# Kernel optimization log

Measured on AMD Instinct MI355X. Metric: run time of the kernel, lower is better.

## Reference

```python
import math
import jax, jax.numpy as jnp
import numpy as np

B, S, D, H, DFF, BASE = 2, 2048, 1024, 16, 4096, 10000.0
HD = D // H  # 64


def setup_inputs() -> dict:
    key = jax.random.key(0)
    ks = jax.random.split(key, 16)
    sc = 0.02
    inp = {
        "x": jax.random.normal(ks[0], (B, S, D), jnp.float32),
        "positions": jnp.arange(S, dtype=jnp.int32),
        "wq": jax.random.normal(ks[1], (D, D), jnp.float32) * sc,
        "bq": jnp.zeros((D,), jnp.float32),
        "wk": jax.random.normal(ks[2], (D, D), jnp.float32) * sc,
        "bk": jnp.zeros((D,), jnp.float32),
        "wv": jax.random.normal(ks[3], (D, D), jnp.float32) * sc,
        "bv": jnp.zeros((D,), jnp.float32),
        "wo": jax.random.normal(ks[4], (D, D), jnp.float32) * sc,
        "bo": jnp.zeros((D,), jnp.float32),
        "phase_bias": jax.random.uniform(ks[5], (H, HD), jnp.float32, -2.0 * math.pi, 0.0),
        "w1": jax.random.normal(ks[6], (D, DFF), jnp.float32) * sc,
        "b1": jnp.zeros((DFF,), jnp.float32),
        "w2": jax.random.normal(ks[7], (DFF, D), jnp.float32) * sc,
        "b2": jnp.zeros((D,), jnp.float32),
        "g1": jnp.ones((D,), jnp.float32),
        "be1": jnp.zeros((D,), jnp.float32),
        "g2": jnp.ones((D,), jnp.float32),
        "be2": jnp.zeros((D,), jnp.float32),
    }
    return inp


def _layernorm(x, g, b):
    mu = jnp.mean(x, -1, keepdims=True)
    var = jnp.mean(jnp.square(x - mu), -1, keepdims=True)
    return (x - mu) / jnp.sqrt(var + 1e-5) * g + b


def _block(x, positions, wq, bq, wk, bk, wv, bv, wo, bo, phase_bias,
           w1, b1, w2, b2, g1, be1, g2, be2):
    # projections -> (B, H, S, HD)
    def heads(w, b):
        return (x @ w + b).reshape(B, S, H, HD).transpose(0, 2, 1, 3)
    q, k, v = heads(wq, bq), heads(wk, bk), heads(wv, bv)

    # PoPE: magnitudes via softplus, phases from position*freq (+ clamped bias for k)
    mu_q = jax.nn.softplus(q)
    mu_k = jax.nn.softplus(k)
    freqs = 1.0 / BASE ** (jnp.arange(HD, dtype=jnp.float32) / HD)      # (HD,)
    pos_ph = positions[:, None].astype(jnp.float32) * freqs[None, :]     # (S, HD)
    q_ph = pos_ph[None, None]                                            # (1,1,S,HD)
    cb = jnp.clip(phase_bias, -2.0 * math.pi, 0.0)
    k_ph = pos_ph[None, None] + cb[None, :, None, :]                     # (1,H,S,HD)
    q_p = jnp.concatenate([mu_q * jnp.cos(q_ph), mu_q * jnp.sin(q_ph)], -1)  # (B,H,S,2HD)
    k_p = jnp.concatenate([mu_k * jnp.cos(k_ph), mu_k * jnp.sin(k_ph)], -1)

    # manual attention with causal mask and softmax1
    scale = 1.0 / math.sqrt(2 * HD)
    scores = jnp.einsum("bhqd,bhkd->bhqk", q_p, k_p) * scale
    causal = jnp.triu(jnp.ones((S, S), bool), 1)
    scores = jnp.where(causal, -jnp.inf, scores)
    m = jnp.max(scores, -1, keepdims=True)  # finite: diagonal always unmasked
    e = jnp.exp(scores - m)
    w = e / (jnp.exp(-m) + jnp.sum(e, -1, keepdims=True))
    attn = jnp.einsum("bhqk,bhkd->bhqd", w, v)
    attn = attn.transpose(0, 2, 1, 3).reshape(B, S, D) @ wo + bo

    h = _layernorm(x + attn, g1, be1)
    ff = jax.nn.relu(h @ w1 + b1) @ w2 + b2
    return _layernorm(h + ff, g2, be2)


def reference(x, positions, wq, bq, wk, bk, wv, bv, wo, bo, phase_bias,
              w1, b1, w2, b2, g1, be1, g2, be2):
    return _block(x, positions, wq, bq, wk, bk, wv, bv, wo, bo, phase_bias,
                  w1, b1, w2, b2, g1, be1, g2, be2)
```

## Files before the change

### kernel.cpp

```cpp
#include <hip/hip_runtime.h>
#include <hip/hip_bf16.h>
#include <math.h>

#define NB 2
#define NS 2048
#define ND 1024
#define NH 16
#define NHD 64
#define NDFF 4096

typedef __attribute__((ext_vector_type(4))) float f32x4;
typedef __attribute__((ext_vector_type(8))) short bf16x8;

__device__ __forceinline__ short f2bf(float f) {
  union { float f; unsigned u; } v; v.f = f;
  unsigned r = v.u + 0x7fffu + ((v.u >> 16) & 1u);
  return (short)(r >> 16);
}
__device__ __forceinline__ float bf2f(unsigned short u) {
  union { unsigned u; float f; } v; v.u = ((unsigned)u) << 16; return v.f;
}
__device__ __forceinline__ float softplus_f(float x) {
  return fmaxf(x, 0.f) + log1pf(__expf(-fabsf(x)));
}
__device__ __forceinline__ void gl16(const short* g, short* l) {
  __builtin_amdgcn_global_load_lds(
      (const __attribute__((address_space(1))) void*)g,
      (__attribute__((address_space(3))) void*)l, 16, 0, 0);
}
__device__ __forceinline__ void xcd_map(int& row0, int& col0) {
  const int gx = gridDim.x, gy = gridDim.y;
  const int bid = blockIdx.y * gx + blockIdx.x;
  const int rows_px = gy >> 3;
  const int xcd = bid & 7, l = bid >> 3;
  row0 = (xcd * rows_px + (l % rows_px)) * 128;
  col0 = (l / rows_px) * 128;
}

__global__ __launch_bounds__(256) void k_wt(const float* __restrict__ W,
    short* __restrict__ Wt, int K, int N) {
  __shared__ float t[64][65];
  const int k0 = blockIdx.y * 64, n0 = blockIdx.x * 64;
  for (int i = threadIdx.x; i < 4096; i += 256) {
    const int r = i >> 6, c = i & 63;
    t[r][c] = W[(size_t)(k0 + r) * N + n0 + c];
  }
  __syncthreads();
  for (int i = threadIdx.x; i < 4096; i += 256) {
    const int r = i >> 6, c = i & 63;
    Wt[(size_t)(n0 + r) * K + k0 + c] = f2bf(t[c][r]);
  }
}

__global__ __launch_bounds__(256) void k_xb(const float* __restrict__ x,
    short* __restrict__ xb, int n8) {
  const int i = blockIdx.x * 256 + threadIdx.x;
  if (i >= n8) return;
  const float4 a = ((const float4*)x)[i * 2];
  const float4 b = ((const float4*)x)[i * 2 + 1];
  short tmp[8] = { f2bf(a.x), f2bf(a.y), f2bf(a.z), f2bf(a.w),
                   f2bf(b.x), f2bf(b.y), f2bf(b.z), f2bf(b.w) };
  *(int4*)&xb[(size_t)i * 8] = *(const int4*)tmp;
}

__global__ __launch_bounds__(256) void k_prep_v(const short* __restrict__ vb,
    short* __restrict__ vt) {
  __shared__ short t[64][72];
  const int bh = blockIdx.y, b = bh >> 4, h = bh & 15;
  const int s0 = blockIdx.x * 64;
  for (int i = threadIdx.x; i < 512; i += 256) {
    const int sl = i >> 3, d8 = (i & 7) * 8;
    int4 vv = *(const int4*)&vb[((size_t)(b * NS + s0 + sl) * NH + h) * NHD + d8];
    const short* sp = (const short*)&vv;
#pragma unroll
    for (int j = 0; j < 8; j++) t[d8 + j][sl] = sp[j];
  }
  __syncthreads();
  for (int i = threadIdx.x; i < 512; i += 256) {
    const int d = i >> 3, c8 = (i & 7) * 8;
    *(int4*)&vt[((size_t)bh * 64 + d) * NS + s0 + c8] = *(const int4*)&t[d][c8];
  }
}

__global__ __launch_bounds__(256) void k_pope(const short* __restrict__ qb,
    const short* __restrict__ kb, const int* __restrict__ positions,
    const float* __restrict__ phb, short* __restrict__ qp,
    short* __restrict__ kp) {
  const size_t i8 = ((size_t)blockIdx.x * 256 + threadIdx.x) * 8;
  const int d0 = (int)(i8 & 63);
  const int h  = (int)((i8 >> 6) & 15);
  const int s  = (int)((i8 >> 10) & 2047);
  const int b  = (int)(i8 >> 21);
  const float posf = (float)positions[s];
  int4 qv = *(const int4*)&qb[i8];
  int4 kv = *(const int4*)&kb[i8];
  const short* qs = (const short*)&qv;
  const short* ks = (const short*)&kv;
  short qc[8], qsn[8], kc[8], ksn[8];
#pragma unroll
  for (int j = 0; j < 8; j++) {
    const int d = d0 + j;
    const float freq = __expf(-(float)d * (float)(9.210340371976184 / 64.0));
    const float muq = softplus_f(bf2f((unsigned short)qs[j]));
    const float muk = softplus_f(bf2f((unsigned short)ks[j]));
    float cb = phb[h * 64 + d];
    cb = fminf(fmaxf(cb, -6.283185307179586f), 0.f);
    float snq, csq, snk, csk;
    __sincosf(posf * freq, &snq, &csq);
    __sincosf(posf * freq + cb, &snk, &csk);
    qc[j] = f2bf(muq * csq); qsn[j] = f2bf(muq * snq);
    kc[j] = f2bf(muk * csk); ksn[j] = f2bf(muk * snk);
  }
  const size_t o = (((size_t)(b * 16 + h) * NS + s) * 128) + d0;
  *(int4*)&qp[o] = *(const int4*)qc;
  *(int4*)&qp[o + 64] = *(const int4*)qsn;
  *(int4*)&kp[o] = *(const int4*)kc;
  *(int4*)&kp[o + 64] = *(const int4*)ksn;
}

#define BKK 32

__device__ __forceinline__ void gemm_core(const short* __restrict__ A,
    const short* __restrict__ Wt, const int K, const int kbeg, const int kend,
    const int row0, const int col0, short* lsA, short* lsB, f32x4 acc[4][4]) {
  const int tid = threadIdx.x;
  const int lane = tid & 63, wave = tid >> 6;
  const int lr = lane & 15, lk8 = (lane >> 4) << 3;
  const int wr = wave >> 1, wc = wave & 1;
  const int srow = lane >> 2, scol = (lane & 3) << 3;
  const int wbase = wave * 32;
#pragma unroll
  for (int m = 0; m < 4; m++)
#pragma unroll
    for (int n = 0; n < 4; n++) acc[m][n] = 0.f;
  const short* gA0 = &A[(size_t)(row0 + wbase + srow) * K + scol];
  const short* gA1 = gA0 + (size_t)16 * K;
  const short* gB0 = &Wt[(size_t)(col0 + wbase + srow) * K + scol];
  const short* gB1 = gB0 + (size_t)16 * K;
  short* const lA0 = lsA + wbase * 32;
  short* const lB0 = lsB + wbase * 32;
  auto stage = [&](int buf, int kk) {
    const int o = buf * 4096;
    gl16(gA0 + kk, lA0 + o);
    gl16(gA1 + kk, lA0 + o + 512);
    gl16(gB0 + kk, lB0 + o);
    gl16(gB1 + kk, lB0 + o + 512);
  };
  stage(0, kbeg);
  __syncthreads();
  int cur = 0;
  for (int k0 = kbeg; k0 < kend; k0 += BKK) {
    if (k0 + BKK < kend) stage(cur ^ 1, k0 + BKK);
    const short* la = lsA + cur * 4096;
    const short* lb = lsB + cur * 4096;
    bf16x8 af[4], bf_[4];
#pragma unroll
    for (int m = 0; m < 4; m++)
      af[m] = *(const bf16x8*)&la[(wr * 64 + m * 16 + lr) * 32 + lk8];
#pragma unroll
    for (int n = 0; n < 4; n++)
      bf_[n] = *(const bf16x8*)&lb[(wc * 64 + n * 16 + lr) * 32 + lk8];
#pragma unroll
    for (int m = 0; m < 4; m++)
#pragma unroll
      for (int n = 0; n < 4; n++)
        acc[m][n] = __builtin_amdgcn_mfma_f32_16x16x32_bf16(af[m], bf_[n], acc[m][n], 0, 0, 0);
    __syncthreads();
    cur ^= 1;
  }
}

template<int RELU, int OUTBF16>
__global__ __launch_bounds__(256) void k_gemm(const short* __restrict__ A,
    const short* __restrict__ Wt, const float* __restrict__ bias,
    void* __restrict__ C, int M, int N, int K) {
  __shared__ short lsA[2 * 4096], lsB[2 * 4096];
  f32x4 acc[4][4];
  int row0, col0;
  xcd_map(row0, col0);
  gemm_core(A, Wt, K, 0, K, row0, col0, lsA, lsB, acc);
  const int lane = threadIdx.x & 63, wave = threadIdx.x >> 6;
  const int lr = lane & 15, r4 = (lane >> 4) << 2;
  const int wr = wave >> 1, wc = wave & 1;
#pragma unroll
  for (int m = 0; m < 4; m++) {
#pragma unroll
    for (int n = 0; n < 4; n++) {
      const int col = col0 + wc * 64 + n * 16 + lr;
      const float bv = bias[col];
#pragma unroll
      for (int r = 0; r < 4; r++) {
        const int row = row0 + wr * 64 + m * 16 + r4 + r;
        float val = acc[m][n][r] + bv;
        if (RELU) val = fmaxf(val, 0.f);
        if (OUTBF16) ((short*)C)[(size_t)row * N + col] = f2bf(val);
        else ((float*)C)[(size_t)row * N + col] = val;
      }
    }
  }
}

__global__ __launch_bounds__(256) void k_gemm3(const short* __restrict__ xb,
    const short* __restrict__ wqT, const short* __restrict__ wkT,
    const short* __restrict__ wvT, const float* __restrict__ bq,
    const float* __restrict__ bk, const float* __restrict__ bv,
    short* __restrict__ qb, short* __restrict__ kb, short* __restrict__ vb) {
  __shared__ short lsA[2 * 4096], lsB[2 * 4096];
  const int z = blockIdx.z;
  const short* Wt = (z == 0) ? wqT : (z == 1) ? wkT : wvT;
  const float* bias = (z == 0) ? bq : (z == 1) ? bk : bv;
  short* C = (z == 0) ? qb : (z == 1) ? kb : vb;
  f32x4 acc[4][4];
  int row0, col0;
  xcd_map(row0, col0);
  gemm_core(xb, Wt, ND, 0, ND, row0, col0, lsA, lsB, acc);
  const int lane = threadIdx.x & 63, wave = threadIdx.x >> 6;
  const int lr = lane & 15, r4 = (lane >> 4) << 2;
  const int wr = wave >> 1, wc = wave & 1;
#pragma unroll
  for (int m = 0; m < 4; m++) {
#pragma unroll
    for (int n = 0; n < 4; n++) {
      const int col = col0 + wc * 64 + n * 16 + lr;
      const float bvs = bias[col];
#pragma unroll
      for (int r = 0; r < 4; r++) {
        const int row = row0 + wr * 64 + m * 16 + r4 + r;
        C[(size_t)row * ND + col] = f2bf(acc[m][n][r] + bvs);
      }
    }
  }
}

__global__ __launch_bounds__(256) void k_gemm_sk(const short* __restrict__ A,
    const short* __restrict__ Wt, float* __restrict__ C0, float* __restrict__ C1,
    int M, int N, int K) {
  __shared__ short lsA[2 * 4096], lsB[2 * 4096];
  f32x4 acc[4][4];
  const int z = blockIdx.z;
  const int khalf = K >> 1, kbeg = z * khalf, kend = kbeg + khalf;
  int row0, col0;
  xcd_map(row0, col0);
  gemm_core(A, Wt, K, kbeg, kend, row0, col0, lsA, lsB, acc);
  float* C = z ? C1 : C0;
  const int lane = threadIdx.x & 63, wave = threadIdx.x >> 6;
  const int lr = lane & 15, r4 = (lane >> 4) << 2;
  const int wr = wave >> 1, wc = wave & 1;
#pragma unroll
  for (int m = 0; m < 4; m++) {
#pragma unroll
    for (int n = 0; n < 4; n++) {
      const int col = col0 + wc * 64 + n * 16 + lr;
#pragma unroll
      for (int r = 0; r < 4; r++) {
        const int row = row0 + wr * 64 + m * 16 + r4 + r;
        C[(size_t)row * N + col] = acc[m][n][r];
      }
    }
  }
}

__device__ __forceinline__ void attn_proc(const bf16x8 aq[4], f32x4 acc_o[4],
    float l_p[4], const int rowb, const int kb,
    const short (*kpl)[136], const short (*vl)[72], short (*pl)[72],
    const int lr, const int lk) {
  f32x4 s_acc[4];
#pragma unroll
  for (int n = 0; n < 4; n++) s_acc[n] = 0.f;
#pragma unroll
  for (int ks = 0; ks < 4; ks++) {
    bf16x8 bk_[4];
#pragma unroll
    for (int n = 0; n < 4; n++)
      bk_[n] = *(const bf16x8*)&kpl[n * 16 + lr][ks * 32 + lk * 8];
#pragma unroll
    for (int n = 0; n < 4; n++)
      s_acc[n] = __builtin_amdgcn_mfma_f32_16x16x32_bf16(aq[ks], bk_[n], s_acc[n], 0, 0, 0);
  }
  const float scale = 0.08838834764831845f;
  const bool domask = (kb + 63 > rowb);
#pragma unroll
  for (int n = 0; n < 4; n++) {
#pragma unroll
    for (int r = 0; r < 4; r++) {
      const float sv = s_acc[n][r] * scale;
      float p;
      if (domask) {
        const int rel = rowb + lk * 4 + r - kb;
        p = (n * 16 + lr <= rel) ? __expf(sv) : 0.f;
      } else {
        p = __expf(sv);
      }
      s_acc[n][r] = p;
      l_p[r] += p;
    }
  }
#pragma unroll
  for (int n = 0; n < 4; n++)
#pragma unroll
    for (int r = 0; r < 4; r++)
      pl[lk * 4 + r][n * 16 + lr] = f2bf(s_acc[n][r]);
#pragma unroll
  for (int ks = 0; ks < 2; ks++) {
    const bf16x8 ap = *(const bf16x8*)&pl[lr][ks * 32 + lk * 8];
    bf16x8 bv_[4];
#pragma unroll
    for (int nd = 0; nd < 4; nd++)
      bv_[nd] = *(const bf16x8*)&vl[nd * 16 + lr][ks * 32 + lk * 8];
#pragma unroll
    for (int nd = 0; nd < 4; nd++)
      acc_o[nd] = __builtin_amdgcn_mfma_f32_16x16x32_bf16(ap, bv_[nd], acc_o[nd], 0, 0, 0);
  }
}

__global__ __launch_bounds__(512) void k_attn2(
    const short* __restrict__ qp, const short* __restrict__ kp,
    const short* __restrict__ vt, short* __restrict__ attn) {
  __shared__ short kp_l[2][64][136];
  __shared__ short v_l[2][64][72];
  __shared__ short p_l[8][16][72];
  const int bh = blockIdx.y, b = bh >> 4, h = bh & 15;
  const int tL = blockIdx.x, tH = 15 - tL;
  const int q0L = tL * 128, q0H = tH * 128;
  const int tid = threadIdx.x, wave = tid >> 6, lane = tid & 63;
  const int lr = lane & 15, lk = lane >> 4;

  bf16x8 aqH[4], aqL[4];
  {
    const short* qrH = qp + ((size_t)bh * NS + q0H + wave * 16 + lr) * 128;
    const short* qrL = qp + ((size_t)bh * NS + q0L + wave * 16 + lr) * 128;
#pragma unroll
    for (int ks = 0; ks < 4; ks++) {
      aqH[ks] = *(const bf16x8*)&qrH[ks * 32 + lk * 8];
      aqL[ks] = *(const bf16x8*)&qrL[ks * 32 + lk * 8];
    }
  }
  f32x4 accH[4], accL[4];
  float lH[4], lL[4];
#pragma unroll
  for (int r = 0; r < 4; r++) { lH[r] = 0.f; lL[r] = 0.f; }
#pragma unroll
  for (int n = 0; n < 4; n++) { accH[n] = 0.f; accL[n] = 0.f; }

  const short* kpb = kp + (size_t)bh * NS * 128;
  const short* vtb = vt + (size_t)bh * 64 * NS;
  const int nch = q0H / 64 + 2;
  const int rowbH = q0H + wave * 16, rowbL = q0L + wave * 16;

  const int krow = tid >> 3, kcol = (tid & 7) * 16;
  const int vrow = tid >> 3, vcol = (tid & 7) * 8;

  int4 rk0, rk1, rv;
  {
    const short* s = &kpb[(size_t)krow * 128 + kcol];
    rk0 = ((const int4*)s)[0]; rk1 = ((const int4*)s)[1];
    rv = *(const int4*)&vtb[(size_t)vrow * NS + vcol];
  }
  ((int4*)&kp_l[0][krow][kcol])[0] = rk0;
  ((int4*)&kp_l[0][krow][kcol])[1] = rk1;
  *(int4*)&v_l[0][vrow][vcol] = rv;
  __syncthreads();

  for (int c = 0; c < nch; c++) {
    const int kb = c * 64;
    const int cur = c & 1;
    const bool more = (c + 1) < nch;
    if (more) {
      const int kb2 = kb + 64;
      const short* s = &kpb[(size_t)(kb2 + krow) * 128 + kcol];
      rk0 = ((const int4*)s)[0]; rk1 = ((const int4*)s)[1];
      rv = *(const int4*)&vtb[(size_t)vrow * NS + kb2 + vcol];
    }
    if (rowbH + 15 >= kb)
      attn_proc(aqH, accH, lH, rowbH, kb, kp_l[cur], v_l[cur], p_l[wave], lr, lk);
    if (rowbL + 15 >= kb)
      attn_proc(aqL, accL, lL, rowbL, kb, kp_l[cur], v_l[cur], p_l[wave], lr, lk);
    if (more) {
      ((int4*)&kp_l[cur ^ 1][krow][kcol])[0] = rk0;
      ((int4*)&kp_l[cur ^ 1][krow][kcol])[1] = rk1;
      *(int4*)&v_l[cur ^ 1][vrow][vcol] = rv;
    }
    __syncthreads();
  }
#pragma unroll
  for (int r = 0; r < 4; r++) {
    float sH = lH[r], sL = lL[r];
#pragma unroll
    for (int off = 8; off; off >>= 1) {
      sH += __shfl_xor(sH, off);
      sL += __shfl_xor(sL, off);
    }
    lH[r] = 1.f / (1.f + sH);
    lL[r] = 1.f / (1.f + sL);
  }
#pragma unroll
  for (int nd = 0; nd < 4; nd++) {
#pragma unroll
    for (int r = 0; r < 4; r++) {
      const int d = nd * 16 + lr;
      const int rowH = q0H + wave * 16 + lk * 4 + r;
      const int rowL = q0L + wave * 16 + lk * 4 + r;
      attn[(((size_t)b * NS + rowH) * NH + h) * NHD + d] = f2bf(accH[nd][r] * lH[r]);
      attn[(((size_t)b * NS + rowL) * NH + h) * NHD + d] = f2bf(accL[nd][r] * lL[r]);
    }
  }
}

template<int RBF16, int OUTBF16>
__global__ __launch_bounds__(256) void k_ln3(const float* __restrict__ A0,
    const float* __restrict__ A1, const float* __restrict__ badd,
    const void* __restrict__ Rv, const float* __restrict__ g,
    const float* __restrict__ be, void* __restrict__ out) {
  const int row = blockIdx.x, tid = threadIdx.x;
  const float4 a0 = ((const float4*)(A0 + (size_t)row * ND))[tid];
  const float4 a1 = ((const float4*)(A1 + (size_t)row * ND))[tid];
  const float4 bd = ((const float4*)badd)[tid];
  float r0, r1, r2, r3;
  if (RBF16) {
    short4 rr = *(const short4*)((const short*)Rv + (size_t)row * ND + tid * 4);
    r0 = bf2f((unsigned short)rr.x); r1 = bf2f((unsigned short)rr.y);
    r2 = bf2f((unsigned short)rr.z); r3 = bf2f((unsigned short)rr.w);
  } else {
    const float4 rr = ((const float4*)((const float*)Rv + (size_t)row * ND))[tid];
    r0 = rr.x; r1 = rr.y; r2 = rr.z; r3 = rr.w;
  }
  const float x0 = a0.x + a1.x + bd.x + r0;
  const float x1 = a0.y + a1.y + bd.y + r1;
  const float x2 = a0.z + a1.z + bd.z + r2;
  const float x3 = a0.w + a1.w + bd.w + r3;
  float s = x0 + x1 + x2 + x3;
  float sq = x0 * x0 + x1 * x1 + x2 * x2 + x3 * x3;
#pragma unroll
  for (int off = 32; off; off >>= 1) {
    s += __shfl_xor(s, off);
    sq += __shfl_xor(sq, off);
  }
  __shared__ float ss[4], ssq[4];
  const int wave = tid >> 6, lane = tid & 63;
  if (lane == 0) { ss[wave] = s; ssq[wave] = sq; }
  __syncthreads();
  s = ss[0] + ss[1] + ss[2] + ss[3];
  sq = ssq[0] + ssq[1] + ssq[2] + ssq[3];
  const float mu = s * (1.f / (float)ND);
  const float var = sq * (1.f / (float)ND) - mu * mu;
  const float rstd = rsqrtf(var + 1e-5f);
  const float4 gg = ((const float4*)g)[tid];
  const float4 bb = ((const float4*)be)[tid];
  const float o0 = (x0 - mu) * rstd * gg.x + bb.x;
  const float o1 = (x1 - mu) * rstd * gg.y + bb.y;
  const float o2 = (x2 - mu) * rstd * gg.z + bb.z;
  const float o3 = (x3 - mu) * rstd * gg.w + bb.w;
  if (OUTBF16) {
    short4 ov = { f2bf(o0), f2bf(o1), f2bf(o2), f2bf(o3) };
    *(short4*)((short*)out + (size_t)row * ND + tid * 4) = ov;
  } else {
    float4 ov = { o0, o1, o2, o3 };
    ((float4*)((float*)out + (size_t)row * ND))[tid] = ov;
  }
}

extern "C" void kernel_launch(void* const* d_in, const int* in_sizes, int n_in,
                              void* d_out, int out_size, void* d_ws, size_t ws_size,
                              hipStream_t stream) {
  const float* x   = (const float*)d_in[0];
  const int*   pos = (const int*)d_in[1];
  const float* wq  = (const float*)d_in[2];
  const float* bq  = (const float*)d_in[3];
  const float* wk  = (const float*)d_in[4];
  const float* bk  = (const float*)d_in[5];
  const float* wv  = (const float*)d_in[6];
  const float* bv  = (const float*)d_in[7];
  const float* wo  = (const float*)d_in[8];
  const float* bo  = (const float*)d_in[9];
  const float* phb = (const float*)d_in[10];
  const float* w1  = (const float*)d_in[11];
  const float* b1  = (const float*)d_in[12];
  const float* w2  = (const float*)d_in[13];
  const float* b2  = (const float*)d_in[14];
  const float* g1  = (const float*)d_in[15];
  const float* be1 = (const float*)d_in[16];
  const float* g2  = (const float*)d_in[17];
  const float* be2 = (const float*)d_in[18];

  char* ws = (char*)d_ws;
  const size_t MB = 1024 * 1024;
  if (ws_size < 112 * MB) return;
  short* qb     = (short*)(ws + 0 * MB);
  short* kb     = (short*)(ws + 8 * MB);
  short* vb     = (short*)(ws + 16 * MB);
  short* qp     = (short*)(ws + 24 * MB);
  short* kp     = (short*)(ws + 40 * MB);
  short* vt     = (short*)(ws + 56 * MB);
  short* xb     = (short*)(ws + 64 * MB);
  short* attnb  = (short*)(ws + 72 * MB);
  float* attnC0 = (float*)(ws + 0 * MB);
  float* attnC1 = (float*)(ws + 24 * MB);
  short* hb     = (short*)(ws + 16 * MB);
  short* ffh    = (short*)(ws + 40 * MB);
  float* ffC0   = (float*)(ws + 72 * MB);
  float* ffC1   = (float*)(ws + 0 * MB);
  short* wqT    = (short*)(ws + 88 * MB);
  short* wkT    = (short*)(ws + 90 * MB);
  short* wvT    = (short*)(ws + 92 * MB);
  short* woT    = (short*)(ws + 94 * MB);
  short* w1T    = (short*)(ws + 96 * MB);
  short* w2T    = (short*)(ws + 104 * MB);

  dim3 blk(256);
  k_wt<<<dim3(16, 16), blk, 0, stream>>>(wq, wqT, ND, ND);
  k_wt<<<dim3(16, 16), blk, 0, stream>>>(wk, wkT, ND, ND);
  k_wt<<<dim3(16, 16), blk, 0, stream>>>(wv, wvT, ND, ND);
  k_wt<<<dim3(16, 16), blk, 0, stream>>>(wo, woT, ND, ND);
  k_wt<<<dim3(64, 16), blk, 0, stream>>>(w1, w1T, ND, NDFF);
  k_wt<<<dim3(16, 64), blk, 0, stream>>>(w2, w2T, NDFF, ND);
  k_xb<<<dim3((NB * NS * ND / 8 + 255) / 256), blk, 0, stream>>>(x, xb, NB * NS * ND / 8);
  k_gemm3<<<dim3(ND / 128, (NB * NS) / 128, 3), blk, 0, stream>>>(
      xb, wqT, wkT, wvT, bq, bk, bv, qb, kb, vb);
  k_pope<<<dim3(NB * NS * ND / 8 / 256), blk, 0, stream>>>(qb, kb, pos, phb, qp, kp);
  k_prep_v<<<dim3(NS / 64, NB * NH), blk, 0, stream>>>(vb, vt);
  k_attn2<<<dim3(8, NB * NH), dim3(512), 0, stream>>>(qp, kp, vt, attnb);
  k_gemm_sk<<<dim3(ND / 128, (NB * NS) / 128, 2), blk, 0, stream>>>(
      attnb, woT, attnC0, attnC1, NB * NS, ND, ND);
  k_ln3<0, 1><<<dim3(NB * NS), blk, 0, stream>>>(attnC0, attnC1, bo, x, g1, be1, hb);
  k_gemm<1, 1><<<dim3(NDFF / 128, (NB * NS) / 128), blk, 0, stream>>>(
      hb, w1T, b1, ffh, NB * NS, NDFF, ND);
  k_gemm_sk<<<dim3(ND / 128, (NB * NS) / 128, 2), blk, 0, stream>>>(
      ffh, w2T, ffC0, ffC1, NB * NS, ND, NDFF);
  k_ln3<1, 0><<<dim3(NB * NS), blk, 0, stream>>>(ffC0, ffC1, b2, hb, g2, be2, (float*)d_out);
}
```

Before: 295.6 us.

## Split attention into 64-row tile pairs per block and merge weight transposes

The attention kernel now gives each 512-thread block two 64-row query tiles (a heavy and a light one, paired for causal balance), with four waves each instead of two 128-row tiles per wave pair. This doubles the grid to 512 blocks and halves per-wave register state, aiming for better occupancy and load balance. The trade-off is that K/V chunks are now loaded by twice as many blocks. The six weight-transpose launches are also merged into a single launch to cut launch overhead.

```diff
diff --git a/kernel.cpp b/kernel.cpp
--- a/kernel.cpp
+++ b/kernel.cpp
@@ -37,10 +37,27 @@
   col0 = (l / rows_px) * 128;
 }
 
-__global__ __launch_bounds__(256) void k_wt(const float* __restrict__ W,
-    short* __restrict__ Wt, int K, int N) {
+__global__ __launch_bounds__(256) void k_wt6(
+    const float* __restrict__ wq, const float* __restrict__ wk,
+    const float* __restrict__ wv, const float* __restrict__ wo,
+    const float* __restrict__ w1, const float* __restrict__ w2,
+    short* __restrict__ wqT, short* __restrict__ wkT, short* __restrict__ wvT,
+    short* __restrict__ woT, short* __restrict__ w1T, short* __restrict__ w2T) {
   __shared__ float t[64][65];
-  const int k0 = blockIdx.y * 64, n0 = blockIdx.x * 64;
+  const int bid = blockIdx.x;
+  const float* W; short* Wt; int K, N, local;
+  if (bid < 1024) {
+    const int wsel = bid >> 8; local = bid & 255;
+    W  = wsel == 0 ? wq  : wsel == 1 ? wk  : wsel == 2 ? wv  : wo;
+    Wt = wsel == 0 ? wqT : wsel == 1 ? wkT : wsel == 2 ? wvT : woT;
+    K = ND; N = ND;
+  } else if (bid < 2048) {
+    local = bid - 1024; W = w1; Wt = w1T; K = ND; N = NDFF;
+  } else {
+    local = bid - 2048; W = w2; Wt = w2T; K = NDFF; N = ND;
+  }
+  const int nx = N >> 6;
+  const int n0 = (local % nx) * 64, k0 = (local / nx) * 64;
   for (int i = threadIdx.x; i < 4096; i += 256) {
     const int r = i >> 6, c = i & 63;
     t[r][c] = W[(size_t)(k0 + r) * N + n0 + c];
@@ -313,40 +330,37 @@
   }
 }
 
-__global__ __launch_bounds__(512) void k_attn2(
+__global__ __launch_bounds__(512) void k_attn3(
     const short* __restrict__ qp, const short* __restrict__ kp,
     const short* __restrict__ vt, short* __restrict__ attn) {
   __shared__ short kp_l[2][64][136];
   __shared__ short v_l[2][64][72];
   __shared__ short p_l[8][16][72];
   const int bh = blockIdx.y, b = bh >> 4, h = bh & 15;
-  const int tL = blockIdx.x, tH = 15 - tL;
-  const int q0L = tL * 128, q0H = tH * 128;
+  const int bx = blockIdx.x;
   const int tid = threadIdx.x, wave = tid >> 6, lane = tid & 63;
   const int lr = lane & 15, lk = lane >> 4;
-
-  bf16x8 aqH[4], aqL[4];
+  const int tHeavy = 31 - bx;
+  const int myTile = (wave < 4) ? tHeavy : bx;
+  const int rowb = myTile * 64 + (wave & 3) * 16;
+  const int nch = tHeavy + 1;
+
+  bf16x8 aq[4];
   {
-    const short* qrH = qp + ((size_t)bh * NS + q0H + wave * 16 + lr) * 128;
-    const short* qrL = qp + ((size_t)bh * NS + q0L + wave * 16 + lr) * 128;
-#pragma unroll
-    for (int ks = 0; ks < 4; ks++) {
-      aqH[ks] = *(const bf16x8*)&qrH[ks * 32 + lk * 8];
-      aqL[ks] = *(const bf16x8*)&qrL[ks * 32 + lk * 8];
-    }
-  }
-  f32x4 accH[4], accL[4];
-  float lH[4], lL[4];
-#pragma unroll
-  for (int r = 0; r < 4; r++) { lH[r] = 0.f; lL[r] = 0.f; }
-#pragma unroll
-  for (int n = 0; n < 4; n++) { accH[n] = 0.f; accL[n] = 0.f; }
+    const short* qrow = qp + ((size_t)bh * NS + rowb + lr) * 128;
+#pragma unroll
+    for (int ks = 0; ks < 4; ks++)
+      aq[ks] = *(const bf16x8*)&qrow[ks * 32 + lk * 8];
+  }
+  f32x4 acc[4];
+  float lsum[4];
+#pragma unroll
+  for (int r = 0; r < 4; r++) lsum[r] = 0.f;
+#pragma unroll
+  for (int n = 0; n < 4; n++) acc[n] = 0.f;
 
   const short* kpb = kp + (size_t)bh * NS * 128;
   const short* vtb = vt + (size_t)bh * 64 * NS;
-  const int nch = q0H / 64 + 2;
-  const int rowbH = q0H + wave * 16, rowbL = q0L + wave * 16;
-
   const int krow = tid >> 3, kcol = (tid & 7) * 16;
   const int vrow = tid >> 3, vcol = (tid & 7) * 8;
 
@@ -371,10 +385,8 @@
       rk0 = ((const int4*)s)[0]; rk1 = ((const int4*)s)[1];
       rv = *(const int4*)&vtb[(size_t)vrow * NS + kb2 + vcol];
     }
-    if (rowbH + 15 >= kb)
-      attn_proc(aqH, accH, lH, rowbH, kb, kp_l[cur], v_l[cur], p_l[wave], lr, lk);
-    if (rowbL + 15 >= kb)
-      attn_proc(aqL, accL, lL, rowbL, kb, kp_l[cur], v_l[cur], p_l[wave], lr, lk);
+    if (rowb + 15 >= kb)
+      attn_proc(aq, acc, lsum, rowb, kb, kp_l[cur], v_l[cur], p_l[wave], lr, lk);
     if (more) {
       ((int4*)&kp_l[cur ^ 1][krow][kcol])[0] = rk0;
       ((int4*)&kp_l[cur ^ 1][krow][kcol])[1] = rk1;
@@ -384,24 +396,18 @@
   }
 #pragma unroll
   for (int r = 0; r < 4; r++) {
-    float sH = lH[r], sL = lL[r];
-#pragma unroll
-    for (int off = 8; off; off >>= 1) {
-      sH += __shfl_xor(sH, off);
-      sL += __shfl_xor(sL, off);
-    }
-    lH[r] = 1.f / (1.f + sH);
-    lL[r] = 1.f / (1.f + sL);
+    float s = lsum[r];
+#pragma unroll
+    for (int off = 8; off; off >>= 1) s += __shfl_xor(s, off);
+    lsum[r] = 1.f / (1.f + s);
   }
 #pragma unroll
   for (int nd = 0; nd < 4; nd++) {
 #pragma unroll
     for (int r = 0; r < 4; r++) {
       const int d = nd * 16 + lr;
-      const int rowH = q0H + wave * 16 + lk * 4 + r;
-      const int rowL = q0L + wave * 16 + lk * 4 + r;
-      attn[(((size_t)b * NS + rowH) * NH + h) * NHD + d] = f2bf(accH[nd][r] * lH[r]);
-      attn[(((size_t)b * NS + rowL) * NH + h) * NHD + d] = f2bf(accL[nd][r] * lL[r]);
+      const int row = rowb + lk * 4 + r;
+      attn[(((size_t)b * NS + row) * NH + h) * NHD + d] = f2bf(acc[nd][r] * lsum[r]);
     }
   }
 }
@@ -507,18 +513,14 @@
   short* w2T    = (short*)(ws + 104 * MB);
 
   dim3 blk(256);
-  k_wt<<<dim3(16, 16), blk, 0, stream>>>(wq, wqT, ND, ND);
-  k_wt<<<dim3(16, 16), blk, 0, stream>>>(wk, wkT, ND, ND);
-  k_wt<<<dim3(16, 16), blk, 0, stream>>>(wv, wvT, ND, ND);
-  k_wt<<<dim3(16, 16), blk, 0, stream>>>(wo, woT, ND, ND);
-  k_wt<<<dim3(64, 16), blk, 0, stream>>>(w1, w1T, ND, NDFF);
-  k_wt<<<dim3(16, 64), blk, 0, stream>>>(w2, w2T, NDFF, ND);
+  k_wt6<<<dim3(3072), blk, 0, stream>>>(wq, wk, wv, wo, w1, w2,
+                                        wqT, wkT, wvT, woT, w1T, w2T);
   k_xb<<<dim3((NB * NS * ND / 8 + 255) / 256), blk, 0, stream>>>(x, xb, NB * NS * ND / 8);
   k_gemm3<<<dim3(ND / 128, (NB * NS) / 128, 3), blk, 0, stream>>>(
       xb, wqT, wkT, wvT, bq, bk, bv, qb, kb, vb);
   k_pope<<<dim3(NB * NS * ND / 8 / 256), blk, 0, stream>>>(qb, kb, pos, phb, qp, kp);
   k_prep_v<<<dim3(NS / 64, NB * NH), blk, 0, stream>>>(vb, vt);
-  k_attn2<<<dim3(8, NB * NH), dim3(512), 0, stream>>>(qp, kp, vt, attnb);
+  k_attn3<<<dim3(16, NB * NH), dim3(512), 0, stream>>>(qp, kp, vt, attnb);
   k_gemm_sk<<<dim3(ND / 128, (NB * NS) / 128, 2), blk, 0, stream>>>(
       attnb, woT, attnC0, attnC1, NB * NS, ND, ND);
   k_ln3<0, 1><<<dim3(NB * NS), blk, 0, stream>>>(attnC0, attnC1, bo, x, g1, be1, hb);
```

Result: faster. 278.6 us (-5.7%).
